# Optimization experiments

Measured on AMD Instinct MI355X. Metric: run time of the kernel, lower is better.

## Reference

```python
import jax, jax.numpy as jnp
import numpy as np

N_NODES = 50000
N_EDGES = 800000
IN_F = 64
D_ATT = 64
HEADS = 8
D_HEAD = D_ATT // HEADS  # 8


def segment_softmax(logits, seg, num_segments):
    # logits: [E, d]; seg: [E] int segment ids
    m = jax.ops.segment_max(logits, seg, num_segments=num_segments)  # [N, d]
    m = jnp.where(jnp.isfinite(m), m, 0.0)  # guard empty segments
    e = jnp.exp(logits - m[seg])
    s = jax.ops.segment_sum(e, seg, num_segments=num_segments)  # [N, d]
    return e / (s[seg] + 1e-16)


def setup_inputs() -> dict:
    key = jax.random.key(0)
    ks = jax.random.split(key, 8)
    x = jax.random.normal(ks[0], (N_NODES, IN_F), dtype=jnp.float32)
    edge = jax.random.randint(ks[1], (2, N_EDGES), 0, N_NODES, dtype=jnp.int32)
    sc = 1.0 / np.sqrt(IN_F).astype(np.float32)
    Wq = jax.random.normal(ks[2], (IN_F, D_ATT), dtype=jnp.float32) * sc
    Wk = jax.random.normal(ks[3], (IN_F, D_ATT), dtype=jnp.float32) * sc
    Wv = jax.random.normal(ks[4], (IN_F, D_ATT), dtype=jnp.float32) * sc
    bq = jnp.zeros((D_ATT,), jnp.float32)
    bk = jnp.zeros((D_ATT,), jnp.float32)
    bv = jnp.zeros((D_ATT,), jnp.float32)
    return {"x": x, "Wq": Wq, "bq": bq, "Wk": Wk, "bk": bk, "Wv": Wv, "bv": bv, "edge": edge}


def reference(x, Wq, bq, Wk, bk, Wv, bv, edge):
    # Linear projections then split heads: [N, H, D_HEAD]
    q = (x @ Wq + bq).reshape(-1, HEADS, D_HEAD)
    k = (x @ Wk + bk).reshape(-1, HEADS, D_HEAD)
    v = (x @ Wv + bv).reshape(-1, HEADS, D_HEAD)
    src = q[edge[0]]      # [E, H, D_HEAD]
    dst_k = k[edge[1]]    # [E, H, D_HEAD]
    # Faithful to source: sum over dim=1 (the HEAD axis) -> [E, D_HEAD]
    prods = jnp.sum(src * dst_k, axis=1) / np.float32(np.sqrt(D_HEAD))
    # segment softmax grouped by edge[attention_norm_idx] (= edge[1])
    attention = segment_softmax(prods, edge[1], N_NODES)
    return attention, v, prods
```

## Files before the change

kernel.cpp:

```cpp
#include <hip/hip_runtime.h>
#include <hip/hip_bf16.h>
#include <hip/hip_fp16.h>

#define N_NODES 50000
#define N_EDGES 800000

typedef __attribute__((ext_vector_type(4))) unsigned int uint4v;
typedef __attribute__((ext_vector_type(2))) float f32x2;

static __device__ __forceinline__ float bfu_lo(unsigned int u) {
    union { unsigned int u; float f; } v; v.u = u << 16; return v.f;
}
static __device__ __forceinline__ float bfu_hi(unsigned int u) {
    union { unsigned int u; float f; } v; v.u = u & 0xffff0000u; return v.f;
}
static __device__ __forceinline__ unsigned short f2bf(float f) {
    union { float f; unsigned int u; } v; v.f = f;
    v.u += 0x7fffu + ((v.u >> 16) & 1u);
    return (unsigned short)(v.u >> 16);
}

__global__ __launch_bounds__(256, 2)
void proj_qkv(const float* __restrict__ x,
              const float* __restrict__ Wq, const float* __restrict__ bq,
              const float* __restrict__ Wk, const float* __restrict__ bk,
              const float* __restrict__ Wv, const float* __restrict__ bv,
              unsigned short* __restrict__ Qb, unsigned short* __restrict__ Kb,
              float* __restrict__ V, unsigned int* __restrict__ ssum_u)
{
    __shared__ float xs[32 * 64];
    const int tid  = threadIdx.x;
    const int c    = tid & 63;
    const int w    = tid >> 6;
    const int row0 = blockIdx.x * 32;
    const int nrows = min(32, N_NODES - row0);

    {
        const int z = blockIdx.x * 256 + tid;
        if (z < N_NODES * 4) ssum_u[z] = 0u;
    }

    {
        const float4* xg  = (const float4*)(x + (size_t)row0 * 64);
        float4*       xs4 = (float4*)xs;
        const int nf4 = nrows * 16;
        for (int i = tid; i < nf4; i += 256) xs4[i] = xg[i];
    }
    __syncthreads();

    const int r0 = w * 8;

    float accq[8], acck[8], accv[8];
    {
        const float bqc = bq[c], bkc = bk[c], bvc = bv[c];
#pragma unroll
        for (int i = 0; i < 8; ++i) { accq[i] = bqc; acck[i] = bkc; accv[i] = bvc; }
    }

    for (int jc = 0; jc < 8; ++jc) {
        float wq[8], wk[8], wv[8];
#pragma unroll
        for (int j = 0; j < 8; ++j) {
            const int row = (jc * 8 + j) * 64 + c;
            wq[j] = Wq[row]; wk[j] = Wk[row]; wv[j] = Wv[row];
        }
#pragma unroll
        for (int i = 0; i < 8; ++i) {
            const float4* xr = (const float4*)(xs + (r0 + i) * 64 + jc * 8);
            const float4 xv0 = xr[0], xv1 = xr[1];
            accq[i] += xv0.x * wq[0] + xv0.y * wq[1] + xv0.z * wq[2] + xv0.w * wq[3]
                     + xv1.x * wq[4] + xv1.y * wq[5] + xv1.z * wq[6] + xv1.w * wq[7];
            acck[i] += xv0.x * wk[0] + xv0.y * wk[1] + xv0.z * wk[2] + xv0.w * wk[3]
                     + xv1.x * wk[4] + xv1.y * wk[5] + xv1.z * wk[6] + xv1.w * wk[7];
            accv[i] += xv0.x * wv[0] + xv0.y * wv[1] + xv0.z * wv[2] + xv0.w * wv[3]
                     + xv1.x * wv[4] + xv1.y * wv[5] + xv1.z * wv[6] + xv1.w * wv[7];
        }
    }

    const int ocqk = (c & 7) * 8 + (c >> 3);
#pragma unroll
    for (int i = 0; i < 8; ++i) {
        const int r = r0 + i;
        if (r < nrows) {
            const size_t o = (size_t)(row0 + r) * 64;
            Qb[o + ocqk] = f2bf(accq[i]);
            Kb[o + ocqk] = f2bf(acck[i]);
            __builtin_nontemporal_store(accv[i], V + o + c);
        }
    }
}

__global__ __launch_bounds__(256)
void edge_kernel(const unsigned short* __restrict__ Qb,
                 const unsigned short* __restrict__ Kb,
                 const int* __restrict__ edge,
                 float* __restrict__ prods, __half2* __restrict__ ssum)
{
    const int gid = blockIdx.x * 256 + threadIdx.x;
    const int e2 = gid >> 2;
    const int dp = gid & 3;
    const int eA = e2 * 2;

    const int2 esrc = *(const int2*)(edge + eA);
    const int2 edst = *(const int2*)(edge + N_EDGES + eA);

    const uint4v* qA = (const uint4v*)(Qb + (size_t)esrc.x * 64 + dp * 16);
    const uint4v* kA = (const uint4v*)(Kb + (size_t)edst.x * 64 + dp * 16);
    const uint4v* qB = (const uint4v*)(Qb + (size_t)esrc.y * 64 + dp * 16);
    const uint4v* kB = (const uint4v*)(Kb + (size_t)edst.y * 64 + dp * 16);
    const uint4v qA0 = qA[0], qA1 = qA[1];
    const uint4v kA0 = kA[0], kA1 = kA[1];
    const uint4v qB0 = qB[0], qB1 = qB[1];
    const uint4v kB0 = kB[0], kB1 = kB[1];

    float sA0 = 0.f, sA1 = 0.f, sB0 = 0.f, sB1 = 0.f;
#pragma unroll
    for (int i = 0; i < 4; ++i) {
        sA0 += bfu_lo(qA0[i]) * bfu_lo(kA0[i]) + bfu_hi(qA0[i]) * bfu_hi(kA0[i]);
        sA1 += bfu_lo(qA1[i]) * bfu_lo(kA1[i]) + bfu_hi(qA1[i]) * bfu_hi(kA1[i]);
        sB0 += bfu_lo(qB0[i]) * bfu_lo(kB0[i]) + bfu_hi(qB0[i]) * bfu_hi(kB0[i]);
        sB1 += bfu_lo(qB1[i]) * bfu_lo(kB1[i]) + bfu_hi(qB1[i]) * bfu_hi(kB1[i]);
    }

    const float c = 0.35355339059327373f;
    const float pA0 = sA0 * c, pA1 = sA1 * c;
    const float pB0 = sB0 * c, pB1 = sB1 * c;
    *(f32x2*)(prods + (size_t)eA * 8 + dp * 2)       = (f32x2){pA0, pA1};
    *(f32x2*)(prods + (size_t)(eA + 1) * 8 + dp * 2) = (f32x2){pB0, pB1};
    unsafeAtomicAdd(ssum + (size_t)edst.x * 4 + dp,
                    __floats2half2_rn(__expf(pA0), __expf(pA1)));
    unsafeAtomicAdd(ssum + (size_t)edst.y * 4 + dp,
                    __floats2half2_rn(__expf(pB0), __expf(pB1)));
}

__global__ __launch_bounds__(256)
void norm_kernel(const int* __restrict__ edge,
                 const float* __restrict__ prods,
                 const __half2* __restrict__ ssum, float* __restrict__ att)
{
    const int gid = blockIdx.x * 256 + threadIdx.x;
    const int e2 = gid >> 2;
    const int dp = gid & 3;
    const int eA = e2 * 2;

    const int2 edst = *(const int2*)(edge + N_EDGES + eA);

    const f32x2 pA = *(const f32x2*)(prods + (size_t)eA * 8 + dp * 2);
    const f32x2 pB = *(const f32x2*)(prods + (size_t)(eA + 1) * 8 + dp * 2);
    const __half2 sA = ssum[(size_t)edst.x * 4 + dp];
    const __half2 sB = ssum[(size_t)edst.y * 4 + dp];

    f32x2 rA, rB;
    rA.x = __expf(pA.x) / (__low2float(sA)  + 1e-16f);
    rA.y = __expf(pA.y) / (__high2float(sA) + 1e-16f);
    rB.x = __expf(pB.x) / (__low2float(sB)  + 1e-16f);
    rB.y = __expf(pB.y) / (__high2float(sB) + 1e-16f);
    __builtin_nontemporal_store(rA, (f32x2*)(att + (size_t)eA * 8 + dp * 2));
    __builtin_nontemporal_store(rB, (f32x2*)(att + (size_t)(eA + 1) * 8 + dp * 2));
}

extern "C" void kernel_launch(void* const* d_in, const int* in_sizes, int n_in,
                              void* d_out, int out_size, void* d_ws, size_t ws_size,
                              hipStream_t stream)
{
    const float* x    = (const float*)d_in[0];
    const float* Wq   = (const float*)d_in[1];
    const float* bq   = (const float*)d_in[2];
    const float* Wk   = (const float*)d_in[3];
    const float* bk   = (const float*)d_in[4];
    const float* Wv   = (const float*)d_in[5];
    const float* bv   = (const float*)d_in[6];
    const int*   edge = (const int*)d_in[7];

    float* out   = (float*)d_out;
    float* att   = out;
    float* V     = out + 6400000;
    float* prods = out + 9600000;

    unsigned short* Qb = (unsigned short*)d_ws;
    unsigned short* Kb = Qb + 3200000;
    __half2*        ssum = (__half2*)(Kb + 3200000);

    proj_qkv<<<(N_NODES + 31) / 32, 256, 0, stream>>>(
        x, Wq, bq, Wk, bk, Wv, bv, Qb, Kb, V, (unsigned int*)ssum);

    const int nwork = N_EDGES * 2;
    edge_kernel<<<nwork / 256, 256, 0, stream>>>(Qb, Kb, edge, prods, ssum);
    norm_kernel<<<nwork / 256, 256, 0, stream>>>(edge, prods, ssum, att);
}
```

Before: 170.8 us.

## Partition Q/K and softmax sums into per-slice planes with slice-major edge scheduling

Q and K are stored as four separate planes, each holding 16 bf16 values per node, and the softmax denominators get one plane per slice. The edge pass assigns each block a single slice, so the gathered data for that slice (about 1.6 MB per plane) can stay cache resident while blocks sweep the edges. Products go to a slice-major scratch buffer, and a per-edge normalise kernel later writes both prods and att as full rows. This adds a scratch round trip and a workspace-size check with a fallback path in exchange for better gather locality.

```diff
diff --git a/kernel.cpp b/kernel.cpp
--- a/kernel.cpp
+++ b/kernel.cpp
@@ -7,6 +7,13 @@
 
 typedef __attribute__((ext_vector_type(4))) unsigned int uint4v;
 typedef __attribute__((ext_vector_type(2))) float f32x2;
+typedef __attribute__((ext_vector_type(4))) float f32x4;
+typedef __attribute__((ext_vector_type(2))) int   i32x2;
+
+#define SLICE_U 800000
+#define SSUM_SLICE 50000
+#define SCR_SLICE 1600000
+#define WS_NEEDED 39200000u
 
 static __device__ __forceinline__ float bfu_lo(unsigned int u) {
     union { unsigned int u; float f; } v; v.u = u << 16; return v.f;
@@ -77,37 +84,43 @@
         }
     }
 
-    const int ocqk = (c & 7) * 8 + (c >> 3);
+    const int dpc = (c & 7) >> 1;
+    const int oc  = (c & 1) * 8 + (c >> 3);
+    const size_t tb = (size_t)dpc * SLICE_U;
 #pragma unroll
     for (int i = 0; i < 8; ++i) {
         const int r = r0 + i;
         if (r < nrows) {
-            const size_t o = (size_t)(row0 + r) * 64;
-            Qb[o + ocqk] = f2bf(accq[i]);
-            Kb[o + ocqk] = f2bf(acck[i]);
-            __builtin_nontemporal_store(accv[i], V + o + c);
+            const size_t node = (size_t)(row0 + r);
+            Qb[tb + node * 16 + oc] = f2bf(accq[i]);
+            Kb[tb + node * 16 + oc] = f2bf(acck[i]);
+            __builtin_nontemporal_store(accv[i], V + node * 64 + c);
         }
     }
 }
 
 __global__ __launch_bounds__(256)
-void edge_kernel(const unsigned short* __restrict__ Qb,
-                 const unsigned short* __restrict__ Kb,
-                 const int* __restrict__ edge,
-                 float* __restrict__ prods, __half2* __restrict__ ssum)
-{
-    const int gid = blockIdx.x * 256 + threadIdx.x;
-    const int e2 = gid >> 2;
-    const int dp = gid & 3;
-    const int eA = e2 * 2;
-
-    const int2 esrc = *(const int2*)(edge + eA);
-    const int2 edst = *(const int2*)(edge + N_EDGES + eA);
-
-    const uint4v* qA = (const uint4v*)(Qb + (size_t)esrc.x * 64 + dp * 16);
-    const uint4v* kA = (const uint4v*)(Kb + (size_t)edst.x * 64 + dp * 16);
-    const uint4v* qB = (const uint4v*)(Qb + (size_t)esrc.y * 64 + dp * 16);
-    const uint4v* kB = (const uint4v*)(Kb + (size_t)edst.y * 64 + dp * 16);
+void edge_part(const unsigned short* __restrict__ Qb,
+               const unsigned short* __restrict__ Kb,
+               const int* __restrict__ edge,
+               float* __restrict__ scratch, __half2* __restrict__ ssum)
+{
+    const int b = blockIdx.x;
+    const int dp = (b & 7) >> 1;
+    const int chunk = (b >> 3) * 2 + (b & 1);
+    const int p = chunk * 256 + threadIdx.x;
+    if (p >= N_EDGES / 2) return;
+    const int eA = p * 2;
+
+    const i32x2 esrc = __builtin_nontemporal_load((const i32x2*)(edge + eA));
+    const i32x2 edst = __builtin_nontemporal_load((const i32x2*)(edge + N_EDGES + eA));
+
+    const unsigned short* Qs = Qb + (size_t)dp * SLICE_U;
+    const unsigned short* Ks = Kb + (size_t)dp * SLICE_U;
+    const uint4v* qA = (const uint4v*)(Qs + (size_t)esrc.x * 16);
+    const uint4v* kA = (const uint4v*)(Ks + (size_t)edst.x * 16);
+    const uint4v* qB = (const uint4v*)(Qs + (size_t)esrc.y * 16);
+    const uint4v* kB = (const uint4v*)(Ks + (size_t)edst.y * 16);
     const uint4v qA0 = qA[0], qA1 = qA[1];
     const uint4v kA0 = kA[0], kA1 = kA[1];
     const uint4v qB0 = qB[0], qB1 = qB[1];
@@ -122,33 +135,111 @@
         sB1 += bfu_lo(qB1[i]) * bfu_lo(kB1[i]) + bfu_hi(qB1[i]) * bfu_hi(kB1[i]);
     }
 
-    const float c = 0.35355339059327373f;
-    const float pA0 = sA0 * c, pA1 = sA1 * c;
-    const float pB0 = sB0 * c, pB1 = sB1 * c;
-    *(f32x2*)(prods + (size_t)eA * 8 + dp * 2)       = (f32x2){pA0, pA1};
-    *(f32x2*)(prods + (size_t)(eA + 1) * 8 + dp * 2) = (f32x2){pB0, pB1};
-    unsafeAtomicAdd(ssum + (size_t)edst.x * 4 + dp,
+    const float cc = 0.35355339059327373f;
+    const float pA0 = sA0 * cc, pA1 = sA1 * cc;
+    const float pB0 = sB0 * cc, pB1 = sB1 * cc;
+    __builtin_nontemporal_store((f32x4){pA0, pA1, pB0, pB1},
+        (f32x4*)(scratch + (size_t)dp * SCR_SLICE + (size_t)p * 4));
+    unsafeAtomicAdd(ssum + (size_t)dp * SSUM_SLICE + edst.x,
                     __floats2half2_rn(__expf(pA0), __expf(pA1)));
-    unsafeAtomicAdd(ssum + (size_t)edst.y * 4 + dp,
+    unsafeAtomicAdd(ssum + (size_t)dp * SSUM_SLICE + edst.y,
                     __floats2half2_rn(__expf(pB0), __expf(pB1)));
 }
 
 __global__ __launch_bounds__(256)
-void norm_kernel(const int* __restrict__ edge,
-                 const float* __restrict__ prods,
-                 const __half2* __restrict__ ssum, float* __restrict__ att)
+void norm_part(const int* __restrict__ edge, const float* __restrict__ scratch,
+               const __half2* __restrict__ ssum,
+               float* __restrict__ att, float* __restrict__ prods)
+{
+    const int e = blockIdx.x * 256 + threadIdx.x;
+    const int dst = edge[N_EDGES + e];
+
+    const f32x2 p0 = *(const f32x2*)(scratch + 0 * SCR_SLICE + (size_t)e * 2);
+    const f32x2 p1 = *(const f32x2*)(scratch + 1 * SCR_SLICE + (size_t)e * 2);
+    const f32x2 p2 = *(const f32x2*)(scratch + 2 * SCR_SLICE + (size_t)e * 2);
+    const f32x2 p3 = *(const f32x2*)(scratch + 3 * SCR_SLICE + (size_t)e * 2);
+    const __half2 s0 = ssum[0 * SSUM_SLICE + dst];
+    const __half2 s1 = ssum[1 * SSUM_SLICE + dst];
+    const __half2 s2 = ssum[2 * SSUM_SLICE + dst];
+    const __half2 s3 = ssum[3 * SSUM_SLICE + dst];
+
+    __builtin_nontemporal_store((f32x4){p0.x, p0.y, p1.x, p1.y},
+                                (f32x4*)(prods + (size_t)e * 8));
+    __builtin_nontemporal_store((f32x4){p2.x, p2.y, p3.x, p3.y},
+                                (f32x4*)(prods + (size_t)e * 8 + 4));
+
+    f32x4 a0, a1;
+    a0.x = __expf(p0.x) / (__low2float(s0)  + 1e-16f);
+    a0.y = __expf(p0.y) / (__high2float(s0) + 1e-16f);
+    a0.z = __expf(p1.x) / (__low2float(s1)  + 1e-16f);
+    a0.w = __expf(p1.y) / (__high2float(s1) + 1e-16f);
+    a1.x = __expf(p2.x) / (__low2float(s2)  + 1e-16f);
+    a1.y = __expf(p2.y) / (__high2float(s2) + 1e-16f);
+    a1.z = __expf(p3.x) / (__low2float(s3)  + 1e-16f);
+    a1.w = __expf(p3.y) / (__high2float(s3) + 1e-16f);
+    __builtin_nontemporal_store(a0, (f32x4*)(att + (size_t)e * 8));
+    __builtin_nontemporal_store(a1, (f32x4*)(att + (size_t)e * 8 + 4));
+}
+
+__global__ __launch_bounds__(256)
+void edge_fb(const unsigned short* __restrict__ Qb,
+             const unsigned short* __restrict__ Kb,
+             const int* __restrict__ edge,
+             float* __restrict__ prods, __half2* __restrict__ ssum)
 {
     const int gid = blockIdx.x * 256 + threadIdx.x;
     const int e2 = gid >> 2;
     const int dp = gid & 3;
     const int eA = e2 * 2;
 
-    const int2 edst = *(const int2*)(edge + N_EDGES + eA);
-
+    const i32x2 esrc = *(const i32x2*)(edge + eA);
+    const i32x2 edst = *(const i32x2*)(edge + N_EDGES + eA);
+
+    const unsigned short* Qs = Qb + (size_t)dp * SLICE_U;
+    const unsigned short* Ks = Kb + (size_t)dp * SLICE_U;
+    const uint4v* qA = (const uint4v*)(Qs + (size_t)esrc.x * 16);
+    const uint4v* kA = (const uint4v*)(Ks + (size_t)edst.x * 16);
+    const uint4v* qB = (const uint4v*)(Qs + (size_t)esrc.y * 16);
+    const uint4v* kB = (const uint4v*)(Ks + (size_t)edst.y * 16);
+    const uint4v qA0 = qA[0], qA1 = qA[1];
+    const uint4v kA0 = kA[0], kA1 = kA[1];
+    const uint4v qB0 = qB[0], qB1 = qB[1];
+    const uint4v kB0 = kB[0], kB1 = kB[1];
+
+    float sA0 = 0.f, sA1 = 0.f, sB0 = 0.f, sB1 = 0.f;
+#pragma unroll
+    for (int i = 0; i < 4; ++i) {
+        sA0 += bfu_lo(qA0[i]) * bfu_lo(kA0[i]) + bfu_hi(qA0[i]) * bfu_hi(kA0[i]);
+        sA1 += bfu_lo(qA1[i]) * bfu_lo(kA1[i]) + bfu_hi(qA1[i]) * bfu_hi(kA1[i]);
+        sB0 += bfu_lo(qB0[i]) * bfu_lo(kB0[i]) + bfu_hi(qB0[i]) * bfu_hi(kB0[i]);
+        sB1 += bfu_lo(qB1[i]) * bfu_lo(kB1[i]) + bfu_hi(qB1[i]) * bfu_hi(kB1[i]);
+    }
+
+    const float cc = 0.35355339059327373f;
+    const float pA0 = sA0 * cc, pA1 = sA1 * cc;
+    const float pB0 = sB0 * cc, pB1 = sB1 * cc;
+    *(f32x2*)(prods + (size_t)eA * 8 + dp * 2)       = (f32x2){pA0, pA1};
+    *(f32x2*)(prods + (size_t)(eA + 1) * 8 + dp * 2) = (f32x2){pB0, pB1};
+    unsafeAtomicAdd(ssum + (size_t)dp * SSUM_SLICE + edst.x,
+                    __floats2half2_rn(__expf(pA0), __expf(pA1)));
+    unsafeAtomicAdd(ssum + (size_t)dp * SSUM_SLICE + edst.y,
+                    __floats2half2_rn(__expf(pB0), __expf(pB1)));
+}
+
+__global__ __launch_bounds__(256)
+void norm_fb(const int* __restrict__ edge, const float* __restrict__ prods,
+             const __half2* __restrict__ ssum, float* __restrict__ att)
+{
+    const int gid = blockIdx.x * 256 + threadIdx.x;
+    const int e2 = gid >> 2;
+    const int dp = gid & 3;
+    const int eA = e2 * 2;
+
+    const i32x2 edst = *(const i32x2*)(edge + N_EDGES + eA);
     const f32x2 pA = *(const f32x2*)(prods + (size_t)eA * 8 + dp * 2);
     const f32x2 pB = *(const f32x2*)(prods + (size_t)(eA + 1) * 8 + dp * 2);
-    const __half2 sA = ssum[(size_t)edst.x * 4 + dp];
-    const __half2 sB = ssum[(size_t)edst.y * 4 + dp];
+    const __half2 sA = ssum[(size_t)dp * SSUM_SLICE + edst.x];
+    const __half2 sB = ssum[(size_t)dp * SSUM_SLICE + edst.y];
 
     f32x2 rA, rB;
     rA.x = __expf(pA.x) / (__low2float(sA)  + 1e-16f);
@@ -180,11 +271,18 @@
     unsigned short* Qb = (unsigned short*)d_ws;
     unsigned short* Kb = Qb + 3200000;
     __half2*        ssum = (__half2*)(Kb + 3200000);
+    float*          scratch = (float*)(ssum + 200000);
 
     proj_qkv<<<(N_NODES + 31) / 32, 256, 0, stream>>>(
         x, Wq, bq, Wk, bk, Wv, bv, Qb, Kb, V, (unsigned int*)ssum);
 
-    const int nwork = N_EDGES * 2;
-    edge_kernel<<<nwork / 256, 256, 0, stream>>>(Qb, Kb, edge, prods, ssum);
-    norm_kernel<<<nwork / 256, 256, 0, stream>>>(edge, prods, ssum, att);
-}
+    if (ws_size >= (size_t)WS_NEEDED) {
+        edge_part<<<6272, 256, 0, stream>>>(Qb, Kb, edge, scratch, ssum);
+        norm_part<<<N_EDGES / 256, 256, 0, stream>>>(edge, scratch, ssum, att,
+                                                     prods);
+    } else {
+        const int nwork = N_EDGES * 2;
+        edge_fb<<<nwork / 256, 256, 0, stream>>>(Qb, Kb, edge, prods, ssum);
+        norm_fb<<<nwork / 256, 256, 0, stream>>>(edge, prods, ssum, att);
+    }
+}
```

New measurement: 315.8 us. 1.85x slower.

## Fuse projection, edge and normalization kernels into one cooperative persistent kernel

Applied to the files above, without the earlier changes.

Replaces the three separate launches with a single cooperative kernel of 1024 blocks that grid-strides over projection tiles, edge dot-products and the normalization pass, separated by grid-wide syncs. The goal is to remove launch gaps and tail effects between kernels. It trades these for the cost of two grid barriers and lower per-phase parallelism, since the persistent grid is smaller than the original launches. The old three-kernel path remains as a fallback if the cooperative launch fails.

```diff
diff --git a/kernel.cpp b/kernel.cpp
--- a/kernel.cpp
+++ b/kernel.cpp
@@ -1,12 +1,19 @@
 #include <hip/hip_runtime.h>
+#include <hip/hip_cooperative_groups.h>
 #include <hip/hip_bf16.h>
 #include <hip/hip_fp16.h>
 
+namespace cg = cooperative_groups;
+
 #define N_NODES 50000
 #define N_EDGES 800000
 
 typedef __attribute__((ext_vector_type(4))) unsigned int uint4v;
 typedef __attribute__((ext_vector_type(2))) float f32x2;
+typedef __attribute__((ext_vector_type(2))) int   i32x2;
+
+#define NTILES ((N_NODES + 31) / 32)
+#define EDGEWORK (N_EDGES * 2)
 
 static __device__ __forceinline__ float bfu_lo(unsigned int u) {
     union { unsigned int u; float f; } v; v.u = u << 16; return v.f;
@@ -18,6 +25,145 @@
     union { float f; unsigned int u; } v; v.f = f;
     v.u += 0x7fffu + ((v.u >> 16) & 1u);
     return (unsigned short)(v.u >> 16);
+}
+
+__global__ __launch_bounds__(256, 4)
+void fused_gat(const float* __restrict__ x,
+               const float* __restrict__ Wq, const float* __restrict__ bq,
+               const float* __restrict__ Wk, const float* __restrict__ bk,
+               const float* __restrict__ Wv, const float* __restrict__ bv,
+               const int* __restrict__ edge,
+               unsigned short* __restrict__ Qb, unsigned short* __restrict__ Kb,
+               float* __restrict__ V, __half2* __restrict__ ssum,
+               float* __restrict__ prods, float* __restrict__ att)
+{
+    __shared__ float xs[32 * 64];
+    const int tid  = threadIdx.x;
+    const int gtid = blockIdx.x * 256 + tid;
+    const int gtot = gridDim.x * 256;
+
+    {
+        unsigned int* ssum_u = (unsigned int*)ssum;
+        for (int z = gtid; z < N_NODES * 4; z += gtot) ssum_u[z] = 0u;
+
+        const int c = tid & 63;
+        const int w = tid >> 6;
+        const int r0 = w * 8;
+        const float bqc = bq[c], bkc = bk[c], bvc = bv[c];
+        const int ocqk = (c & 7) * 8 + (c >> 3);
+
+        for (int tile = blockIdx.x; tile < NTILES; tile += gridDim.x) {
+            const int row0 = tile * 32;
+            const int nrows = min(32, N_NODES - row0);
+
+            __syncthreads();
+            {
+                const float4* xg  = (const float4*)(x + (size_t)row0 * 64);
+                float4*       xs4 = (float4*)xs;
+                const int nf4 = nrows * 16;
+                for (int i = tid; i < nf4; i += 256) xs4[i] = xg[i];
+            }
+            __syncthreads();
+
+            float accq[8], acck[8], accv[8];
+#pragma unroll
+            for (int i = 0; i < 8; ++i) { accq[i] = bqc; acck[i] = bkc; accv[i] = bvc; }
+
+            for (int jc = 0; jc < 8; ++jc) {
+                float wq[8], wk[8], wv[8];
+#pragma unroll
+                for (int j = 0; j < 8; ++j) {
+                    const int row = (jc * 8 + j) * 64 + c;
+                    wq[j] = Wq[row]; wk[j] = Wk[row]; wv[j] = Wv[row];
+                }
+#pragma unroll
+                for (int i = 0; i < 8; ++i) {
+                    const float4* xr = (const float4*)(xs + (r0 + i) * 64 + jc * 8);
+                    const float4 xv0 = xr[0], xv1 = xr[1];
+                    accq[i] += xv0.x * wq[0] + xv0.y * wq[1] + xv0.z * wq[2] + xv0.w * wq[3]
+                             + xv1.x * wq[4] + xv1.y * wq[5] + xv1.z * wq[6] + xv1.w * wq[7];
+                    acck[i] += xv0.x * wk[0] + xv0.y * wk[1] + xv0.z * wk[2] + xv0.w * wk[3]
+                             + xv1.x * wk[4] + xv1.y * wk[5] + xv1.z * wk[6] + xv1.w * wk[7];
+                    accv[i] += xv0.x * wv[0] + xv0.y * wv[1] + xv0.z * wv[2] + xv0.w * wv[3]
+                             + xv1.x * wv[4] + xv1.y * wv[5] + xv1.z * wv[6] + xv1.w * wv[7];
+                }
+            }
+
+#pragma unroll
+            for (int i = 0; i < 8; ++i) {
+                const int r = r0 + i;
+                if (r < nrows) {
+                    const size_t o = (size_t)(row0 + r) * 64;
+                    Qb[o + ocqk] = f2bf(accq[i]);
+                    Kb[o + ocqk] = f2bf(acck[i]);
+                    __builtin_nontemporal_store(accv[i], V + o + c);
+                }
+            }
+        }
+    }
+
+    __threadfence();
+    cg::this_grid().sync();
+
+    for (int g = gtid; g < EDGEWORK; g += gtot) {
+        const int e2 = g >> 2;
+        const int dp = g & 3;
+        const int eA = e2 * 2;
+
+        const i32x2 esrc = *(const i32x2*)(edge + eA);
+        const i32x2 edst = *(const i32x2*)(edge + N_EDGES + eA);
+
+        const uint4v* qA = (const uint4v*)(Qb + (size_t)esrc.x * 64 + dp * 16);
+        const uint4v* kA = (const uint4v*)(Kb + (size_t)edst.x * 64 + dp * 16);
+        const uint4v* qB = (const uint4v*)(Qb + (size_t)esrc.y * 64 + dp * 16);
+        const uint4v* kB = (const uint4v*)(Kb + (size_t)edst.y * 64 + dp * 16);
+        const uint4v qA0 = qA[0], qA1 = qA[1];
+        const uint4v kA0 = kA[0], kA1 = kA[1];
+        const uint4v qB0 = qB[0], qB1 = qB[1];
+        const uint4v kB0 = kB[0], kB1 = kB[1];
+
+        float sA0 = 0.f, sA1 = 0.f, sB0 = 0.f, sB1 = 0.f;
+#pragma unroll
+        for (int i = 0; i < 4; ++i) {
+            sA0 += bfu_lo(qA0[i]) * bfu_lo(kA0[i]) + bfu_hi(qA0[i]) * bfu_hi(kA0[i]);
+            sA1 += bfu_lo(qA1[i]) * bfu_lo(kA1[i]) + bfu_hi(qA1[i]) * bfu_hi(kA1[i]);
+            sB0 += bfu_lo(qB0[i]) * bfu_lo(kB0[i]) + bfu_hi(qB0[i]) * bfu_hi(kB0[i]);
+            sB1 += bfu_lo(qB1[i]) * bfu_lo(kB1[i]) + bfu_hi(qB1[i]) * bfu_hi(kB1[i]);
+        }
+
+        const float cc = 0.35355339059327373f;
+        const float pA0 = sA0 * cc, pA1 = sA1 * cc;
+        const float pB0 = sB0 * cc, pB1 = sB1 * cc;
+        *(f32x2*)(prods + (size_t)eA * 8 + dp * 2)       = (f32x2){pA0, pA1};
+        *(f32x2*)(prods + (size_t)(eA + 1) * 8 + dp * 2) = (f32x2){pB0, pB1};
+        unsafeAtomicAdd(ssum + (size_t)edst.x * 4 + dp,
+                        __floats2half2_rn(__expf(pA0), __expf(pA1)));
+        unsafeAtomicAdd(ssum + (size_t)edst.y * 4 + dp,
+                        __floats2half2_rn(__expf(pB0), __expf(pB1)));
+    }
+
+    __threadfence();
+    cg::this_grid().sync();
+
+    for (int g = gtid; g < EDGEWORK; g += gtot) {
+        const int e2 = g >> 2;
+        const int dp = g & 3;
+        const int eA = e2 * 2;
+
+        const i32x2 edst = *(const i32x2*)(edge + N_EDGES + eA);
+        const f32x2 pA = *(const f32x2*)(prods + (size_t)eA * 8 + dp * 2);
+        const f32x2 pB = *(const f32x2*)(prods + (size_t)(eA + 1) * 8 + dp * 2);
+        const __half2 sA = ssum[(size_t)edst.x * 4 + dp];
+        const __half2 sB = ssum[(size_t)edst.y * 4 + dp];
+
+        f32x2 rA, rB;
+        rA.x = __expf(pA.x) / (__low2float(sA)  + 1e-16f);
+        rA.y = __expf(pA.y) / (__high2float(sA) + 1e-16f);
+        rB.x = __expf(pB.x) / (__low2float(sB)  + 1e-16f);
+        rB.y = __expf(pB.y) / (__high2float(sB) + 1e-16f);
+        __builtin_nontemporal_store(rA, (f32x2*)(att + (size_t)eA * 8 + dp * 2));
+        __builtin_nontemporal_store(rB, (f32x2*)(att + (size_t)(eA + 1) * 8 + dp * 2));
+    }
 }
 
 __global__ __launch_bounds__(256, 2)
@@ -39,7 +185,6 @@
         const int z = blockIdx.x * 256 + tid;
         if (z < N_NODES * 4) ssum_u[z] = 0u;
     }
-
     {
         const float4* xg  = (const float4*)(x + (size_t)row0 * 64);
         float4*       xs4 = (float4*)xs;
@@ -49,14 +194,12 @@
     __syncthreads();
 
     const int r0 = w * 8;
-
     float accq[8], acck[8], accv[8];
     {
         const float bqc = bq[c], bkc = bk[c], bvc = bv[c];
 #pragma unroll
         for (int i = 0; i < 8; ++i) { accq[i] = bqc; acck[i] = bkc; accv[i] = bvc; }
     }
-
     for (int jc = 0; jc < 8; ++jc) {
         float wq[8], wk[8], wv[8];
 #pragma unroll
@@ -76,7 +219,6 @@
                      + xv1.x * wv[4] + xv1.y * wv[5] + xv1.z * wv[6] + xv1.w * wv[7];
         }
     }
-
     const int ocqk = (c & 7) * 8 + (c >> 3);
 #pragma unroll
     for (int i = 0; i < 8; ++i) {
@@ -101,8 +243,8 @@
     const int dp = gid & 3;
     const int eA = e2 * 2;
 
-    const int2 esrc = *(const int2*)(edge + eA);
-    const int2 edst = *(const int2*)(edge + N_EDGES + eA);
+    const i32x2 esrc = *(const i32x2*)(edge + eA);
+    const i32x2 edst = *(const i32x2*)(edge + N_EDGES + eA);
 
     const uint4v* qA = (const uint4v*)(Qb + (size_t)esrc.x * 64 + dp * 16);
     const uint4v* kA = (const uint4v*)(Kb + (size_t)edst.x * 64 + dp * 16);
@@ -122,9 +264,9 @@
         sB1 += bfu_lo(qB1[i]) * bfu_lo(kB1[i]) + bfu_hi(qB1[i]) * bfu_hi(kB1[i]);
     }
 
-    const float c = 0.35355339059327373f;
-    const float pA0 = sA0 * c, pA1 = sA1 * c;
-    const float pB0 = sB0 * c, pB1 = sB1 * c;
+    const float cc = 0.35355339059327373f;
+    const float pA0 = sA0 * cc, pA1 = sA1 * cc;
+    const float pB0 = sB0 * cc, pB1 = sB1 * cc;
     *(f32x2*)(prods + (size_t)eA * 8 + dp * 2)       = (f32x2){pA0, pA1};
     *(f32x2*)(prods + (size_t)(eA + 1) * 8 + dp * 2) = (f32x2){pB0, pB1};
     unsafeAtomicAdd(ssum + (size_t)edst.x * 4 + dp,
@@ -143,8 +285,7 @@
     const int dp = gid & 3;
     const int eA = e2 * 2;
 
-    const int2 edst = *(const int2*)(edge + N_EDGES + eA);
-
+    const i32x2 edst = *(const i32x2*)(edge + N_EDGES + eA);
     const f32x2 pA = *(const f32x2*)(prods + (size_t)eA * 8 + dp * 2);
     const f32x2 pB = *(const f32x2*)(prods + (size_t)(eA + 1) * 8 + dp * 2);
     const __half2 sA = ssum[(size_t)edst.x * 4 + dp];
@@ -181,10 +322,18 @@
     unsigned short* Kb = Qb + 3200000;
     __half2*        ssum = (__half2*)(Kb + 3200000);
 
-    proj_qkv<<<(N_NODES + 31) / 32, 256, 0, stream>>>(
-        x, Wq, bq, Wk, bk, Wv, bv, Qb, Kb, V, (unsigned int*)ssum);
-
-    const int nwork = N_EDGES * 2;
-    edge_kernel<<<nwork / 256, 256, 0, stream>>>(Qb, Kb, edge, prods, ssum);
-    norm_kernel<<<nwork / 256, 256, 0, stream>>>(edge, prods, ssum, att);
-}
+    void* args[] = {(void*)&x,  (void*)&Wq, (void*)&bq, (void*)&Wk, (void*)&bk,
+                    (void*)&Wv, (void*)&bv, (void*)&edge,
+                    (void*)&Qb, (void*)&Kb, (void*)&V, (void*)&ssum,
+                    (void*)&prods, (void*)&att};
+    const hipError_t err = hipLaunchCooperativeKernel(
+        fused_gat, dim3(1024), dim3(256), args, 0u, stream);
+
+    if (err != hipSuccess) {
+        proj_qkv<<<(N_NODES + 31) / 32, 256, 0, stream>>>(
+            x, Wq, bq, Wk, bk, Wv, bv, Qb, Kb, V, (unsigned int*)ssum);
+        const int nwork = N_EDGES * 2;
+        edge_kernel<<<nwork / 256, 256, 0, stream>>>(Qb, Kb, edge, prods, ssum);
+        norm_kernel<<<nwork / 256, 256, 0, stream>>>(edge, prods, ssum, att);
+    }
+}
```

Measured after the change: 649.6 us. 280% more time.
